# Optimization experiments

Measured on AMD Instinct MI355X. Metric: run time of the kernel, lower is better.

The kernel has to match this reference:

```python
import jax, jax.numpy as jnp
from jax import lax
import numpy as np

T, K, KEND = 2048, 4, 8
D, H, WD = 100, 256, 300
V, DICT, C = 20000, 700000, 18


def _build_end_indexed(starts, lens, ids, valid):
    # Group gazetteer words by their END position (the step at which the
    # lattice char cell consumes the word memory cell), padded to KEND slots.
    e_ids = np.zeros((T, KEND), np.int32)
    e_start = np.zeros((T, KEND), np.int32)
    e_mask = np.zeros((T, KEND), np.int32)
    cnt = np.zeros(T, np.int64)
    for t in range(T):
        for k in range(K):
            if valid[t, k]:
                e = int(starts[t, k] + lens[t, k] - 1)
                if cnt[e] < KEND:
                    e_ids[e, cnt[e]] = ids[t, k]
                    e_start[e, cnt[e]] = starts[t, k]
                    e_mask[e, cnt[e]] = 1
                    cnt[e] += 1
    return jnp.asarray(e_ids), jnp.asarray(e_start), jnp.asarray(e_mask)


def setup_inputs():
    ks = jax.random.split(jax.random.key(0), 24)
    inputs = jax.random.randint(ks[0], (1, T), 0, V, dtype=jnp.int32)
    rng = np.random.default_rng(0)
    lens = rng.integers(0, 8, size=(T, K))          # word length; valid iff >= 2
    ids = rng.integers(1, DICT, size=(T, K))        # gazetteer word ids
    pos = np.broadcast_to(np.arange(T)[:, None], (T, K))
    # forward direction: word starts at t, ends at t+len-1
    valid_f = (lens >= 2) & (pos + lens - 1 < T)
    fw_ids, fw_start, fw_mask = _build_end_indexed(pos, lens, ids, valid_f)
    # backward direction, expressed in the flipped frame: start' = T-1-(t+len-1)
    starts_b = T - 1 - (pos + lens - 1)
    valid_b = (lens >= 2) & (starts_b >= 0)
    bw_ids, bw_start, bw_mask = _build_end_indexed(starts_b, lens, ids, valid_b)
    s = 0.08
    nrm = lambda k, shape: jax.random.normal(k, shape, jnp.float32) * s
    p = {}
    i = 1
    for pre in ("fw", "bw"):
        p[pre + "_W_ih"] = nrm(ks[i], (D, 3 * H)); i += 1
        p[pre + "_W_hh"] = nrm(ks[i], (H, 3 * H)); i += 1
        p[pre + "_b"] = jnp.zeros((3 * H,), jnp.float32)
        p[pre + "_aW_ih"] = nrm(ks[i], (D, H)); i += 1
        p[pre + "_aW_hh"] = nrm(ks[i], (H, H)); i += 1
        p[pre + "_ab"] = jnp.zeros((H,), jnp.float32)
        p[pre + "_wW_ih"] = nrm(ks[i], (WD, 3 * H)); i += 1
        p[pre + "_wW_hh"] = nrm(ks[i], (H, 3 * H)); i += 1
        p[pre + "_wb"] = jnp.zeros((3 * H,), jnp.float32)
    out = dict(inputs=inputs, fw_ids=fw_ids, fw_start=fw_start, fw_mask=fw_mask,
               bw_ids=bw_ids, bw_start=bw_start, bw_mask=bw_mask, length=T,
               E=nrm(ks[20], (V, D)), word_table=nrm(ks[21], (DICT, WD)),
               W_lin=nrm(ks[22], (2 * H, C)), b_lin=jnp.zeros((C,), jnp.float32))
    out.update(p)
    return out


def _lattice_pass(x, wemb, start, mask, W_ih, W_hh, b, aW_ih, aW_hh, ab, wW_ih, wW_hh, wb):
    # x: [T,D]; wemb: [T,KEND,WD]; start/mask: [T,KEND]
    Tn, Hn = x.shape[0], W_hh.shape[0]

    def step(carry, xs):
        h, c, Hh, Ch = carry                        # Hh/Ch: [T,H] history of char states
        t, xt, we_t, st, m = xs
        mf = m.astype(x.dtype)[:, None]             # [KEND,1]
        hs, cs = Hh[st], Ch[st]                     # char state at each word's start pos
        # WordLSTMCell: c^w = sigmoid(f)*c_start + sigmoid(i)*tanh(g)
        wi, wf, wg = jnp.split(we_t @ wW_ih + hs @ wW_hh + wb, 3, axis=-1)
        cw = jax.nn.sigmoid(wf) * cs + jax.nn.sigmoid(wi) * jnp.tanh(wg)
        # MultiInputLSTMCell char gates
        ii, oo, gg = jnp.split(xt @ W_ih + h @ W_hh + b, 3, axis=-1)
        i_s, o_s, g_t = jax.nn.sigmoid(ii), jax.nn.sigmoid(oo), jnp.tanh(gg)
        # extra input gate per word, then exp-normalization over {i, alphas}
        alpha = jax.nn.sigmoid(xt @ aW_ih + cw @ aW_hh + ab)   # [KEND,H]
        e_i = jnp.exp(i_s)                                      # [H]
        e_a = jnp.exp(alpha) * mf                               # masked slots drop out
        c_merge = (e_i * g_t + (e_a * cw).sum(0)) / (e_i + e_a.sum(0))
        c_plain = (1.0 - i_s) * c + i_s * g_t                   # no-word branch (f = 1-i)
        c_new = jnp.where(jnp.any(m > 0), c_merge, c_plain)
        h_new = o_s * jnp.tanh(c_new)
        return (h_new, c_new, Hh.at[t].set(h_new), Ch.at[t].set(c_new)), h_new

    z = lambda *sh: jnp.zeros(sh, x.dtype)
    init = (z(Hn), z(Hn), z(Tn, Hn), z(Tn, Hn))
    _, hseq = lax.scan(step, init, (jnp.arange(Tn), x, wemb, start, mask))
    return hseq                                      # [T,H]


def reference(inputs, fw_ids, fw_start, fw_mask, bw_ids, bw_start, bw_mask, length, E,
              word_table, W_lin, b_lin,
              fw_W_ih, fw_W_hh, fw_b, fw_aW_ih, fw_aW_hh, fw_ab, fw_wW_ih, fw_wW_hh, fw_wb,
              bw_W_ih, bw_W_hh, bw_b, bw_aW_ih, bw_aW_hh, bw_ab, bw_wW_ih, bw_wW_hh, bw_wb):
    x = E[inputs[0]]                                 # [T,D] char embeddings (batch=1)
    hf = _lattice_pass(x, word_table[fw_ids], fw_start, fw_mask,
                       fw_W_ih, fw_W_hh, fw_b, fw_aW_ih, fw_aW_hh, fw_ab,
                       fw_wW_ih, fw_wW_hh, fw_wb)
    hb = _lattice_pass(x[::-1], word_table[bw_ids], bw_start, bw_mask,
                       bw_W_ih, bw_W_hh, bw_b, bw_aW_ih, bw_aW_hh, bw_ab,
                       bw_wW_ih, bw_wW_hh, bw_wb)[::-1]
    return (jnp.concatenate([hf, hb], axis=-1) @ W_lin + b_lin)[None]  # [1,T,C]
```

## Files before the change

### kernel.cpp

```cpp
#include <hip/hip_runtime.h>
#include <hip/hip_bf16.h>


#define TSEQ 2048
#define KEND 8
#define DEMB 100
#define H    256
#define H3   768
#define WD   300
#define CCLS 18
#define NTH  256

typedef __attribute__((ext_vector_type(8))) short bf16x8;
typedef __attribute__((ext_vector_type(4))) float f32x4;

#define LO_AT  0
#define LO_A1  131072
#define LO_VS  131584
#define LO_UR  133120
#define LO_RC  143872
#define LO_A2  152064
#define LO_AWS 156288
#define LO_MT  160384
#define SMEM_SCAN 160640

__device__ __forceinline__ float sigf(float x) { return 1.0f / (1.0f + expf(-x)); }
__device__ __forceinline__ float bf2f(unsigned u) { return __uint_as_float(u << 16); }
__device__ __forceinline__ unsigned f2bf(float f) {
  union { float f; unsigned u; } x; x.f = f;
  unsigned r = x.u + 0x7fffu + ((x.u >> 16) & 1u);
  return r >> 16;
}

__global__ __launch_bounds__(64) void k_pack(
    const float* __restrict__ W_hh_f, const float* __restrict__ wW_hh_f, const float* __restrict__ aW_hh_f,
    const float* __restrict__ W_hh_b, const float* __restrict__ wW_hh_b, const float* __restrict__ aW_hh_b,
    unsigned short* __restrict__ Wpk)
{
  const int T = blockIdx.x, dir = blockIdx.y;
  const int lane = threadIdx.x;
  const float* Wg = dir ? W_hh_b  : W_hh_f;
  const float* Ww = dir ? wW_hh_b : wW_hh_f;
  const float* Wa = dir ? aW_hh_b : aW_hh_f;
  for (int ks = 0; ks < 8; ++ks) {
    bf16x8 sv;
#pragma unroll
    for (int e = 0; e < 8; ++e) {
      const int k = ks * 32 + (lane >> 4) * 8 + e;
      float f;
      if (T < 96) {
        const int c = T * 16 + (lane & 15);
        f = (c < H3) ? Wg[(size_t)k * H3 + c] : Ww[(size_t)k * H3 + (c - H3)];
      } else {
        const int c = (T - 96) * 16 + (lane & 15);
        f = Wa[(size_t)k * H + c];
      }
      sv[e] = (short)f2bf(f);
    }
    *(bf16x8*)(Wpk + (((size_t)dir * 112 + T) * 8 + ks) * 512 + lane * 8) = sv;
  }
}

__global__ __launch_bounds__(256) void k_embed(
    const int* __restrict__ inputs, const float* __restrict__ E,
    const float* __restrict__ W_ih_f, const float* __restrict__ b_f,
    const float* __restrict__ aW_ih_f, const float* __restrict__ ab_f,
    const float* __restrict__ W_ih_b, const float* __restrict__ b_b,
    const float* __restrict__ aW_ih_b, const float* __restrict__ ab_b,
    __hip_bfloat16* __restrict__ xg, float* __restrict__ xa)
{
  const int t = blockIdx.x, dir = blockIdx.y;
  const int tid = threadIdx.x;
  const float* W_ih = dir ? W_ih_b : W_ih_f;
  const float* bb   = dir ? b_b    : b_f;
  const float* aW   = dir ? aW_ih_b : aW_ih_f;
  const float* ab   = dir ? ab_b   : ab_f;
  const int src = dir ? (TSEQ - 1 - t) : t;

  __shared__ float xr[DEMB];
  if (tid < DEMB) xr[tid] = E[(size_t)inputs[src] * DEMB + tid];
  __syncthreads();

  float a0 = bb[tid], a1 = bb[H + tid], a2 = bb[2 * H + tid], a3 = ab[tid];
  for (int r = 0; r < DEMB; r += 4) {
    const float4 e4 = *reinterpret_cast<const float4*>(&xr[r]);
    const float ev[4] = {e4.x, e4.y, e4.z, e4.w};
#pragma unroll
    for (int kk = 0; kk < 4; ++kk) {
      const float* wp = W_ih + (size_t)(r + kk) * H3 + tid;
      a0 += ev[kk] * wp[0];
      a1 += ev[kk] * wp[H];
      a2 += ev[kk] * wp[2 * H];
      a3 += ev[kk] * aW[(size_t)(r + kk) * H + tid];
    }
  }
  __hip_bfloat16* xgrow = xg + ((size_t)dir * TSEQ + t) * H3;
  xgrow[tid]         = __float2bfloat16(a0);
  xgrow[H + tid]     = __float2bfloat16(a1);
  xgrow[2 * H + tid] = __float2bfloat16(a2);
  xa[((size_t)dir * TSEQ + t) * H + tid] = a3;
}

__global__ __launch_bounds__(256) void k_wordgates(
    const int* __restrict__ fw_ids, const int* __restrict__ fw_mask,
    const int* __restrict__ bw_ids, const int* __restrict__ bw_mask,
    const float* __restrict__ word_table,
    const float* __restrict__ wW_ih_f, const float* __restrict__ wb_f,
    const float* __restrict__ wW_ih_b, const float* __restrict__ wb_b,
    __hip_bfloat16* __restrict__ wg)
{
  const int t = blockIdx.x, dir = blockIdx.y;
  const int tid = threadIdx.x;
  const int* ids = (dir ? bw_ids : fw_ids) + t * KEND;
  const int* msk = (dir ? bw_mask : fw_mask) + t * KEND;
  const float* wW = dir ? wW_ih_b : wW_ih_f;
  const float* wb = dir ? wb_b    : wb_f;

  __shared__ float we[KEND][WD];
  for (int w = 0; w < KEND; ++w) {
    if (msk[w]) {
      const float* src = word_table + (size_t)ids[w] * WD;
      for (int i = tid; i < WD; i += 256) we[w][i] = src[i];
    }
  }
  __syncthreads();

  __hip_bfloat16* out = wg + ((size_t)dir * TSEQ + t) * KEND * H3;
  for (int w = 0; w < KEND; ++w) {
    if (!msk[w]) continue;
    float a0 = wb[tid], a1 = wb[H + tid], a2 = wb[2 * H + tid];
    for (int r = 0; r < WD; r += 4) {
      const float4 e4 = *reinterpret_cast<const float4*>(&we[w][r]);
      const float ev[4] = {e4.x, e4.y, e4.z, e4.w};
#pragma unroll
      for (int kk = 0; kk < 4; ++kk) {
        const float* wp = wW + (size_t)(r + kk) * H3 + tid;
        a0 += ev[kk] * wp[0];
        a1 += ev[kk] * wp[H];
        a2 += ev[kk] * wp[2 * H];
      }
    }
    out[w * H3 + tid]         = __float2bfloat16(a0);
    out[w * H3 + H + tid]     = __float2bfloat16(a1);
    out[w * H3 + 2 * H + tid] = __float2bfloat16(a2);
  }
}

__global__ __launch_bounds__(NTH, 1) void k_scan(
    const __hip_bfloat16* __restrict__ xg, const float* __restrict__ xa,
    const __hip_bfloat16* __restrict__ wgG, float* __restrict__ hseq,
    const int* __restrict__ fw_start, const int* __restrict__ fw_mask,
    const int* __restrict__ bw_start, const int* __restrict__ bw_mask,
    const unsigned short* __restrict__ Wpk,
    unsigned long long* __restrict__ xb, unsigned* __restrict__ xf)
{
  const int gid = blockIdx.x;
  if (gid != 0 && gid != 1 && gid != 8 && gid != 9) return;
  const int dir  = gid & 1;
  const int side = gid >> 3;

  extern __shared__ char smem[];
  unsigned short* A1_16 = (unsigned short*)(smem + LO_A1);
  unsigned short* vS16  = (unsigned short*)(smem + LO_VS);
  unsigned short* ur16  = (unsigned short*)(smem + LO_UR);
  float* ringC = (float*)(smem + LO_RC);
  unsigned short* awS16 = (unsigned short*)(smem + LO_AWS);
  int* metaI = (int*)(smem + LO_MT);

  const int tid  = threadIdx.x;
  const int lane = tid & 63;
  const int wv   = tid >> 6;
  const int lmod = lane & 15;
  const int lgrp = lane >> 4;

  const int* startA = dir ? bw_start : fw_start;
  const int* maskA  = dir ? bw_mask  : fw_mask;
  const char* WpkD = (const char*)(Wpk + (size_t)dir * 112 * 8 * 512);

  unsigned long long* myPay = xb + (size_t)((dir * 2 + side) * 2) * 192;
  const unsigned long long* peerPay = xb + (size_t)((dir * 2 + (side ^ 1)) * 2) * 192;
  unsigned* myFlag   = xf + (dir * 2 + side) * 32;
  unsigned* peerFlag = xf + (dir * 2 + (side ^ 1)) * 32;

  bf16x8 rW[12][8];
  {
    const char* rp = WpkD + (size_t)(side * 48 + wv * 12) * 8192 + lane * 16;
#pragma unroll
    for (int n = 0; n < 12; ++n)
#pragma unroll
      for (int ks = 0; ks < 8; ++ks)
        rW[n][ks] = *(const bf16x8*)(rp + (n * 8 + ks) * 1024);
  }
  for (int o = tid * 16; o < 131072; o += NTH * 16)
    *(uint4*)(smem + LO_AT + o) = *(const uint4*)(WpkD + (size_t)96 * 8192 + o);
  if (tid < 32) *(uint4*)(smem + LO_A1 + tid * 16) = uint4{0, 0, 0, 0};
  for (int o = tid * 16; o < 4224; o += NTH * 16)
    *(uint4*)(smem + LO_A2 + o) = uint4{0, 0, 0, 0};
  for (int o = tid * 16; o < 8192; o += NTH * 16)
    *(uint4*)(smem + LO_RC + o) = uint4{0, 0, 0, 0};

  unsigned nxI = 0, nxO = 0, nxG = 0; float nxA = 0.f;
  unsigned cxI = 0, cxO = 0, cxG = 0; float cxA = 0.f;
  int nmt = 0;
  {
    const unsigned short* xr = (const unsigned short*)(xg + (size_t)dir * TSEQ * H3);
    nxI = xr[tid]; nxO = xr[H + tid]; nxG = xr[2 * H + tid];
    nxA = xa[(size_t)dir * TSEQ * H + tid];
    if (wv == 3) {
      if (lane < 8) nmt = maskA[lane];
      else if (lane < 16) nmt = startA[lane - 8];
    }
  }
  __syncthreads();
  if (wv == 3) {
    int mAll[8], sAll[8];
#pragma unroll
    for (int s = 0; s < 8; ++s) { mAll[s] = __shfl(nmt, s); sAll[s] = __shfl(nmt, 8 + s); }
    if (lane == 0) {
      int n = 0;
      for (int s = 0; s < 8; ++s)
        if (mAll[s]) { metaI[1 + n] = s; metaI[9 + n] = sAll[s]; ++n; }
      metaI[0] = n;
    }
  }
  cxI = nxI; cxO = nxO; cxG = nxG; cxA = nxA;
  __syncthreads();

  for (int t = 0; t < TSEQ; ++t) {
    const int par = t & 1;
    const int* mp = metaI + par * 32;
    const int nw = mp[0];
    const int us7 = (t + 6) % 7;
    unsigned short* stage16 = side ? (ur16 + us7 * 768) : vS16;
    unsigned short* rcv16   = side ? vS16 : (ur16 + us7 * 768);
    int hasL2w = 0;
    for (int w = 0; w < nw; ++w) hasL2w |= (mp[9 + w] == t - 1);

    unsigned short wgv[24];
#pragma unroll
    for (int it = 0; it < 8; ++it) {
      const int u0 = tid + it * NTH;
      if (u0 < nw * 256) {
        const int w = u0 >> 8, j = u0 & 255;
        const int slot = mp[1 + w];
        const unsigned short* wgp =
            (const unsigned short*)wgG + ((size_t)(dir * TSEQ + t) * KEND + slot) * H3 + j;
        wgv[it * 3 + 0] = wgp[0];
        wgv[it * 3 + 1] = wgp[256];
        wgv[it * 3 + 2] = wgp[512];
      }
    }

#pragma unroll
    for (int g = 0; g < 2; ++g) {
      f32x4 acc[6];
#pragma unroll
      for (int n = 0; n < 6; ++n) acc[n] = f32x4{0.f, 0.f, 0.f, 0.f};
#pragma unroll
      for (int ks = 0; ks < 8; ++ks) {
        const bf16x8 av = *(const bf16x8*)(smem + LO_A1 + ks * 64 + lgrp * 16);
#pragma unroll
        for (int n = 0; n < 6; ++n)
          acc[n] = __builtin_amdgcn_mfma_f32_16x16x32_bf16(av, rW[g * 6 + n][ks], acc[n], 0, 0, 0);
      }
      if (lane < 16) {
#pragma unroll
        for (int n = 0; n < 6; ++n)
          stage16[(wv * 12 + g * 6 + n) * 16 + lane] = (unsigned short)f2bf(acc[n][0]);
      }
    }
    __syncthreads();

    if (tid < 192) {
      const unsigned long long q = *(const unsigned long long*)((const char*)stage16 + tid * 8);
      __hip_atomic_store(myPay + par * 192 + tid, q, __ATOMIC_RELAXED, __HIP_MEMORY_SCOPE_AGENT);
    }
    __syncthreads();

    if (tid == 0)
      __hip_atomic_store(myFlag, (unsigned)(t + 1), __ATOMIC_RELAXED, __HIP_MEMORY_SCOPE_AGENT);

    {
      const int tn = (t + 1 < TSEQ) ? t + 1 : TSEQ - 1;
      const unsigned short* xr = (const unsigned short*)(xg + ((size_t)dir * TSEQ + tn) * H3);
      nxI = xr[tid]; nxO = xr[H + tid]; nxG = xr[2 * H + tid];
      nxA = xa[((size_t)dir * TSEQ + tn) * H + tid];
      if (wv == 3) {
        if (lane < 8) nmt = maskA[tn * KEND + lane];
        else if (lane < 16) nmt = startA[tn * KEND + (lane - 8)];
      }
    }
#pragma unroll
    for (int it = 0; it < 8; ++it) {
      const int u0 = tid + it * NTH;
      if (u0 < nw * 256) {
        const int w = u0 >> 8, j = u0 & 255;
        const int s = mp[9 + w];
        if (side == 1 || s != t - 1) {
          const unsigned short* ur = ur16 + (s % 7) * 768;
          const float wi  = bf2f(wgv[it * 3 + 0]) + bf2f(ur[j]);
          const float wf  = bf2f(wgv[it * 3 + 1]) + bf2f(ur[256 + j]);
          const float wgg = bf2f(wgv[it * 3 + 2]) + bf2f(ur[512 + j]);
          const float cs  = ringC[(s & 7) * 256 + j];
          const float cv  = sigf(wf) * cs + sigf(wi) * tanhf(wgg);
          *(unsigned short*)(smem + LO_A2 + w * 528 + j * 2) = (unsigned short)f2bf(cv);
        }
      }
    }
    if (nw > 0) {
      __syncthreads();

      {
        const int r2 = (lmod > 7) ? 7 : lmod;
        f32x4 ac[4];
#pragma unroll
        for (int m = 0; m < 4; ++m) ac[m] = f32x4{0.f, 0.f, 0.f, 0.f};
#pragma unroll
        for (int ks = 0; ks < 8; ++ks) {
          const bf16x8 a2v = *(const bf16x8*)(smem + LO_A2 + r2 * 528 + ks * 64 + lgrp * 16);
#pragma unroll
          for (int m = 0; m < 4; ++m) {
            const bf16x8 b = *(const bf16x8*)(smem + LO_AT + (size_t)(wv * 4 + m) * 8192 + ks * 1024 + lane * 16);
            ac[m] = __builtin_amdgcn_mfma_f32_16x16x32_bf16(a2v, b, ac[m], 0, 0, 0);
          }
        }
#pragma unroll
        for (int m = 0; m < 4; ++m) {
#pragma unroll
          for (int r = 0; r < 4; ++r) {
            const int row = lgrp * 4 + r;
            if (row < nw && mp[9 + row] != t - 1)
              awS16[row * 256 + (wv * 4 + m) * 16 + lmod] = (unsigned short)f2bf(ac[m][r]);
          }
        }
      }
    }

    if (tid == 0) {
      while (__hip_atomic_load(peerFlag, __ATOMIC_RELAXED, __HIP_MEMORY_SCOPE_AGENT) < (unsigned)(t + 1)) {}
    }
    __syncthreads();

    if (tid < 192) {
      const unsigned long long q =
          __hip_atomic_load(peerPay + par * 192 + tid, __ATOMIC_RELAXED, __HIP_MEMORY_SCOPE_AGENT);
      *(unsigned long long*)((char*)rcv16 + tid * 8) = q;
    }
    __syncthreads();

    if (hasL2w) {
      if (side == 0) {
#pragma unroll
        for (int it = 0; it < 8; ++it) {
          const int u0 = tid + it * NTH;
          if (u0 < nw * 256) {
            const int w = u0 >> 8, j = u0 & 255;
            const int s = mp[9 + w];
            if (s == t - 1) {
              const unsigned short* ur = ur16 + (s % 7) * 768;
              const float wi  = bf2f(wgv[it * 3 + 0]) + bf2f(ur[j]);
              const float wf  = bf2f(wgv[it * 3 + 1]) + bf2f(ur[256 + j]);
              const float wgg = bf2f(wgv[it * 3 + 2]) + bf2f(ur[512 + j]);
              const float cs  = ringC[(s & 7) * 256 + j];
              const float cv  = sigf(wf) * cs + sigf(wi) * tanhf(wgg);
              *(unsigned short*)(smem + LO_A2 + w * 528 + j * 2) = (unsigned short)f2bf(cv);
            }
          }
        }
      }
      __syncthreads();

      {
        const int r2 = (lmod > 7) ? 7 : lmod;
        f32x4 ac[4];
#pragma unroll
        for (int m = 0; m < 4; ++m) ac[m] = f32x4{0.f, 0.f, 0.f, 0.f};
#pragma unroll
        for (int ks = 0; ks < 8; ++ks) {
          const bf16x8 a2v = *(const bf16x8*)(smem + LO_A2 + r2 * 528 + ks * 64 + lgrp * 16);
#pragma unroll
          for (int m = 0; m < 4; ++m) {
            const bf16x8 b = *(const bf16x8*)(smem + LO_AT + (size_t)(wv * 4 + m) * 8192 + ks * 1024 + lane * 16);
            ac[m] = __builtin_amdgcn_mfma_f32_16x16x32_bf16(a2v, b, ac[m], 0, 0, 0);
          }
        }
#pragma unroll
        for (int m = 0; m < 4; ++m) {
#pragma unroll
          for (int r = 0; r < 4; ++r) {
            const int row = lgrp * 4 + r;
            if (row < nw && mp[9 + row] == t - 1)
              awS16[row * 256 + (wv * 4 + m) * 16 + lmod] = (unsigned short)f2bf(ac[m][r]);
          }
        }
      }
      __syncthreads();
    }

    {
      const int j = tid;
      const float i_s = sigf(bf2f(cxI) + bf2f(vS16[j]));
      const float o_s = sigf(bf2f(cxO) + bf2f(vS16[256 + j]));
      const float g_t = tanhf(bf2f(cxG) + bf2f(vS16[512 + j]));
      float cnew;
      if (nw > 0) {
        const float e_i = expf(i_s);
        float num = e_i * g_t, den = e_i;
        for (int w = 0; w < nw; ++w) {
          const float a  = sigf(cxA + bf2f(awS16[w * 256 + j]));
          const float ea = expf(a);
          num += ea * bf2f(*(const unsigned short*)(smem + LO_A2 + w * 528 + j * 2));
          den += ea;
        }
        cnew = num / den;
      } else {
        cnew = (1.f - i_s) * ringC[((t - 1) & 7) * 256 + j] + i_s * g_t;
      }
      const float hnew = o_s * tanhf(cnew);
      ringC[(t & 7) * 256 + j] = cnew;
      A1_16[j] = (unsigned short)f2bf(hnew);
      if ((side == 0) == (j < 128))
        hseq[((size_t)dir * TSEQ + t) * H + j] = hnew;
    }
    if (wv == 3) {
      int mAll[8], sAll[8];
#pragma unroll
      for (int s = 0; s < 8; ++s) { mAll[s] = __shfl(nmt, s); sAll[s] = __shfl(nmt, 8 + s); }
      if (lane == 0) {
        int* mq = metaI + ((t + 1) & 1) * 32;
        int n = 0;
        for (int s = 0; s < 8; ++s)
          if (mAll[s]) { mq[1 + n] = s; mq[9 + n] = sAll[s]; ++n; }
        mq[0] = n;
      }
    }
    cxI = nxI; cxO = nxO; cxG = nxG; cxA = nxA;
    __syncthreads();
  }
}

__global__ __launch_bounds__(64) void k_proj(
    const float* __restrict__ hseq, const float* __restrict__ W_lin,
    const float* __restrict__ b_lin, float* __restrict__ out)
{
  const int t = blockIdx.x;
  const int tid = threadIdx.x;
  __shared__ float hrow[2 * H];
  for (int i = tid; i < H; i += 64) {
    hrow[i]     = hseq[(size_t)t * H + i];
    hrow[H + i] = hseq[((size_t)TSEQ + (TSEQ - 1 - t)) * H + i];
  }
  __syncthreads();
  if (tid < CCLS) {
    float acc = b_lin[tid];
    for (int j = 0; j < 2 * H; ++j) acc += hrow[j] * W_lin[(size_t)j * CCLS + tid];
    out[(size_t)t * CCLS + tid] = acc;
  }
}

extern "C" void kernel_launch(void* const* d_in, const int* in_sizes, int n_in,
                              void* d_out, int out_size, void* d_ws, size_t ws_size,
                              hipStream_t stream)
{
  const int* inputs   = (const int*)d_in[0];
  const int* fw_ids   = (const int*)d_in[1];
  const int* fw_start = (const int*)d_in[2];
  const int* fw_mask  = (const int*)d_in[3];
  const int* bw_ids   = (const int*)d_in[4];
  const int* bw_start = (const int*)d_in[5];
  const int* bw_mask  = (const int*)d_in[6];
  const float* E          = (const float*)d_in[8];
  const float* word_table = (const float*)d_in[9];
  const float* W_lin      = (const float*)d_in[10];
  const float* b_lin      = (const float*)d_in[11];
  const float* fw_W_ih  = (const float*)d_in[12];
  const float* fw_W_hh  = (const float*)d_in[13];
  const float* fw_b     = (const float*)d_in[14];
  const float* fw_aW_ih = (const float*)d_in[15];
  const float* fw_aW_hh = (const float*)d_in[16];
  const float* fw_ab    = (const float*)d_in[17];
  const float* fw_wW_ih = (const float*)d_in[18];
  const float* fw_wW_hh = (const float*)d_in[19];
  const float* fw_wb    = (const float*)d_in[20];
  const float* bw_W_ih  = (const float*)d_in[21];
  const float* bw_W_hh  = (const float*)d_in[22];
  const float* bw_b     = (const float*)d_in[23];
  const float* bw_aW_ih = (const float*)d_in[24];
  const float* bw_aW_hh = (const float*)d_in[25];
  const float* bw_ab    = (const float*)d_in[26];
  const float* bw_wW_ih = (const float*)d_in[27];
  const float* bw_wW_hh = (const float*)d_in[28];
  const float* bw_wb    = (const float*)d_in[29];

  char* p = (char*)d_ws;
  __hip_bfloat16* xg = (__hip_bfloat16*)p;  p += (size_t)2 * TSEQ * H3 * 2;
  float* xa   = (float*)p;                  p += (size_t)2 * TSEQ * H * 4;
  float* hseq = (float*)p;                  p += (size_t)2 * TSEQ * H * 4;
  __hip_bfloat16* wg = (__hip_bfloat16*)p;  p += (size_t)2 * TSEQ * KEND * H3 * 2;
  unsigned short* Wpk = (unsigned short*)p; p += (size_t)2 * 112 * 8 * 512 * 2;
  unsigned long long* xb = (unsigned long long*)p; p += (size_t)2 * 2 * 2 * 192 * 8;
  unsigned* xf = (unsigned*)p;              p += 512;

  hipFuncSetAttribute((const void*)k_scan,
                      hipFuncAttributeMaxDynamicSharedMemorySize, SMEM_SCAN);
  hipMemsetAsync(xf, 0, 512, stream);

  k_pack<<<dim3(112, 2), 64, 0, stream>>>(
      fw_W_hh, fw_wW_hh, fw_aW_hh, bw_W_hh, bw_wW_hh, bw_aW_hh, Wpk);
  k_embed<<<dim3(TSEQ, 2), 256, 0, stream>>>(
      inputs, E, fw_W_ih, fw_b, fw_aW_ih, fw_ab, bw_W_ih, bw_b, bw_aW_ih, bw_ab, xg, xa);
  k_wordgates<<<dim3(TSEQ, 2), 256, 0, stream>>>(
      fw_ids, fw_mask, bw_ids, bw_mask, word_table, fw_wW_ih, fw_wb, bw_wW_ih, bw_wb, wg);
  k_scan<<<16, NTH, SMEM_SCAN, stream>>>(
      xg, xa, wg, hseq, fw_start, fw_mask, bw_start, bw_mask, Wpk, xb, xf);
  k_proj<<<TSEQ, 64, 0, stream>>>(hseq, W_lin, b_lin, (float*)d_out);
}
```

Measured before the change: 16.80 ms.

## Replace flag-based cross-block handshake with sequence-tagged payload words

Each payload word now carries the step number in its upper 32 bits, so the receiving block spins on the data words themselves rather than on a separate flag followed by a second read. This removes the staging barrier, the separate flag store and the extra syncthreads. The word-cell work is also split by side: side 1 computes all word cells before waiting on its peer, and side 0 computes the cells it can before waiting. The cost is doubled payload traffic, since each 64-bit word now holds 32 bits of data, plus per-thread spinning on 384 words.

```diff
diff --git a/kernel.cpp b/kernel.cpp
--- a/kernel.cpp
+++ b/kernel.cpp
@@ -152,7 +152,7 @@
     const int* __restrict__ fw_start, const int* __restrict__ fw_mask,
     const int* __restrict__ bw_start, const int* __restrict__ bw_mask,
     const unsigned short* __restrict__ Wpk,
-    unsigned long long* __restrict__ xb, unsigned* __restrict__ xf)
+    unsigned long long* __restrict__ xb)
 {
   const int gid = blockIdx.x;
   if (gid != 0 && gid != 1 && gid != 8 && gid != 9) return;
@@ -177,10 +177,8 @@
   const int* maskA  = dir ? bw_mask  : fw_mask;
   const char* WpkD = (const char*)(Wpk + (size_t)dir * 112 * 8 * 512);
 
-  unsigned long long* myPay = xb + (size_t)((dir * 2 + side) * 2) * 192;
-  const unsigned long long* peerPay = xb + (size_t)((dir * 2 + (side ^ 1)) * 2) * 192;
-  unsigned* myFlag   = xf + (dir * 2 + side) * 32;
-  unsigned* peerFlag = xf + (dir * 2 + (side ^ 1)) * 32;
+  unsigned long long* myPay = xb + (size_t)((dir * 2 + side) * 2) * 384;
+  const unsigned long long* peerPay = xb + (size_t)((dir * 2 + (side ^ 1)) * 2) * 384;
 
   bf16x8 rW[12][8];
   {
@@ -233,8 +231,6 @@
     const int us7 = (t + 6) % 7;
     unsigned short* stage16 = side ? (ur16 + us7 * 768) : vS16;
     unsigned short* rcv16   = side ? vS16 : (ur16 + us7 * 768);
-    int hasL2w = 0;
-    for (int w = 0; w < nw; ++w) hasL2w |= (mp[9 + w] == t - 1);
 
     unsigned short wgv[24];
 #pragma unroll
@@ -263,22 +259,23 @@
         for (int n = 0; n < 6; ++n)
           acc[n] = __builtin_amdgcn_mfma_f32_16x16x32_bf16(av, rW[g * 6 + n][ks], acc[n], 0, 0, 0);
       }
-      if (lane < 16) {
-#pragma unroll
-        for (int n = 0; n < 6; ++n)
-          stage16[(wv * 12 + g * 6 + n) * 16 + lane] = (unsigned short)f2bf(acc[n][0]);
-      }
-    }
-    __syncthreads();
-
-    if (tid < 192) {
-      const unsigned long long q = *(const unsigned long long*)((const char*)stage16 + tid * 8);
-      __hip_atomic_store(myPay + par * 192 + tid, q, __ATOMIC_RELAXED, __HIP_MEMORY_SCOPE_AGENT);
-    }
-    __syncthreads();
-
-    if (tid == 0)
-      __hip_atomic_store(myFlag, (unsigned)(t + 1), __ATOMIC_RELAXED, __HIP_MEMORY_SCOPE_AGENT);
+#pragma unroll
+      for (int n = 0; n < 6; ++n) {
+        const unsigned hb = f2bf(acc[n][0]) & 0xffffu;
+        const unsigned ob = (unsigned)__shfl_down((int)hb, 1) & 0xffffu;
+        if (lane < 16) {
+          const int tix = wv * 12 + g * 6 + n;
+          stage16[tix * 16 + lane] = (unsigned short)hb;
+          if (!(lane & 1)) {
+            const unsigned long long q =
+                ((unsigned long long)(unsigned)(t + 1) << 32) |
+                (unsigned long long)(hb | (ob << 16));
+            __hip_atomic_store(myPay + par * 384 + tix * 8 + (lane >> 1), q,
+                               __ATOMIC_RELAXED, __HIP_MEMORY_SCOPE_AGENT);
+          }
+        }
+      }
+    }
 
     {
       const int tn = (t + 1 < TSEQ) ? t + 1 : TSEQ - 1;
@@ -290,66 +287,39 @@
         else if (lane < 16) nmt = startA[tn * KEND + (lane - 8)];
       }
     }
-#pragma unroll
-    for (int it = 0; it < 8; ++it) {
-      const int u0 = tid + it * NTH;
-      if (u0 < nw * 256) {
-        const int w = u0 >> 8, j = u0 & 255;
-        const int s = mp[9 + w];
-        if (side == 1 || s != t - 1) {
-          const unsigned short* ur = ur16 + (s % 7) * 768;
-          const float wi  = bf2f(wgv[it * 3 + 0]) + bf2f(ur[j]);
-          const float wf  = bf2f(wgv[it * 3 + 1]) + bf2f(ur[256 + j]);
-          const float wgg = bf2f(wgv[it * 3 + 2]) + bf2f(ur[512 + j]);
-          const float cs  = ringC[(s & 7) * 256 + j];
-          const float cv  = sigf(wf) * cs + sigf(wi) * tanhf(wgg);
-          *(unsigned short*)(smem + LO_A2 + w * 528 + j * 2) = (unsigned short)f2bf(cv);
-        }
-      }
-    }
-    if (nw > 0) {
+    __syncthreads();
+
+    if (side == 0) {
+      if (nw > 0) {
+#pragma unroll
+        for (int it = 0; it < 8; ++it) {
+          const int u0 = tid + it * NTH;
+          if (u0 < nw * 256) {
+            const int w = u0 >> 8, j = u0 & 255;
+            const int s = mp[9 + w];
+            if (s != t - 1) {
+              const unsigned short* ur = ur16 + (s % 7) * 768;
+              const float wi  = bf2f(wgv[it * 3 + 0]) + bf2f(ur[j]);
+              const float wf  = bf2f(wgv[it * 3 + 1]) + bf2f(ur[256 + j]);
+              const float wgg = bf2f(wgv[it * 3 + 2]) + bf2f(ur[512 + j]);
+              const float cs  = ringC[(s & 7) * 256 + j];
+              const float cv  = sigf(wf) * cs + sigf(wi) * tanhf(wgg);
+              *(unsigned short*)(smem + LO_A2 + w * 528 + j * 2) = (unsigned short)f2bf(cv);
+            }
+          }
+        }
+      }
+      if (tid < 192) {
+        unsigned long long q;
+        do { q = __hip_atomic_load(peerPay + par * 384 + tid, __ATOMIC_RELAXED, __HIP_MEMORY_SCOPE_AGENT); }
+        while ((unsigned)(q >> 32) != (unsigned)(t + 1));
+        *(unsigned*)((char*)rcv16 + tid * 4) = (unsigned)q;
+        do { q = __hip_atomic_load(peerPay + par * 384 + 192 + tid, __ATOMIC_RELAXED, __HIP_MEMORY_SCOPE_AGENT); }
+        while ((unsigned)(q >> 32) != (unsigned)(t + 1));
+        *(unsigned*)((char*)rcv16 + (192 + tid) * 4) = (unsigned)q;
+      }
       __syncthreads();
-
-      {
-        const int r2 = (lmod > 7) ? 7 : lmod;
-        f32x4 ac[4];
-#pragma unroll
-        for (int m = 0; m < 4; ++m) ac[m] = f32x4{0.f, 0.f, 0.f, 0.f};
-#pragma unroll
-        for (int ks = 0; ks < 8; ++ks) {
-          const bf16x8 a2v = *(const bf16x8*)(smem + LO_A2 + r2 * 528 + ks * 64 + lgrp * 16);
-#pragma unroll
-          for (int m = 0; m < 4; ++m) {
-            const bf16x8 b = *(const bf16x8*)(smem + LO_AT + (size_t)(wv * 4 + m) * 8192 + ks * 1024 + lane * 16);
-            ac[m] = __builtin_amdgcn_mfma_f32_16x16x32_bf16(a2v, b, ac[m], 0, 0, 0);
-          }
-        }
-#pragma unroll
-        for (int m = 0; m < 4; ++m) {
-#pragma unroll
-          for (int r = 0; r < 4; ++r) {
-            const int row = lgrp * 4 + r;
-            if (row < nw && mp[9 + row] != t - 1)
-              awS16[row * 256 + (wv * 4 + m) * 16 + lmod] = (unsigned short)f2bf(ac[m][r]);
-          }
-        }
-      }
-    }
-
-    if (tid == 0) {
-      while (__hip_atomic_load(peerFlag, __ATOMIC_RELAXED, __HIP_MEMORY_SCOPE_AGENT) < (unsigned)(t + 1)) {}
-    }
-    __syncthreads();
-
-    if (tid < 192) {
-      const unsigned long long q =
-          __hip_atomic_load(peerPay + par * 192 + tid, __ATOMIC_RELAXED, __HIP_MEMORY_SCOPE_AGENT);
-      *(unsigned long long*)((char*)rcv16 + tid * 8) = q;
-    }
-    __syncthreads();
-
-    if (hasL2w) {
-      if (side == 0) {
+      if (nw > 0) {
 #pragma unroll
         for (int it = 0; it < 8; ++it) {
           const int u0 = tid + it * NTH;
@@ -367,32 +337,80 @@
             }
           }
         }
-      }
-      __syncthreads();
-
-      {
-        const int r2 = (lmod > 7) ? 7 : lmod;
-        f32x4 ac[4];
-#pragma unroll
-        for (int m = 0; m < 4; ++m) ac[m] = f32x4{0.f, 0.f, 0.f, 0.f};
-#pragma unroll
-        for (int ks = 0; ks < 8; ++ks) {
-          const bf16x8 a2v = *(const bf16x8*)(smem + LO_A2 + r2 * 528 + ks * 64 + lgrp * 16);
-#pragma unroll
-          for (int m = 0; m < 4; ++m) {
-            const bf16x8 b = *(const bf16x8*)(smem + LO_AT + (size_t)(wv * 4 + m) * 8192 + ks * 1024 + lane * 16);
-            ac[m] = __builtin_amdgcn_mfma_f32_16x16x32_bf16(a2v, b, ac[m], 0, 0, 0);
+        __syncthreads();
+        {
+          const int r2 = (lmod > 7) ? 7 : lmod;
+          f32x4 ac[4];
+#pragma unroll
+          for (int m = 0; m < 4; ++m) ac[m] = f32x4{0.f, 0.f, 0.f, 0.f};
+#pragma unroll
+          for (int ks = 0; ks < 8; ++ks) {
+            const bf16x8 a2v = *(const bf16x8*)(smem + LO_A2 + r2 * 528 + ks * 64 + lgrp * 16);
+#pragma unroll
+            for (int m = 0; m < 4; ++m) {
+              const bf16x8 b = *(const bf16x8*)(smem + LO_AT + (size_t)(wv * 4 + m) * 8192 + ks * 1024 + lane * 16);
+              ac[m] = __builtin_amdgcn_mfma_f32_16x16x32_bf16(a2v, b, ac[m], 0, 0, 0);
+            }
           }
-        }
-#pragma unroll
-        for (int m = 0; m < 4; ++m) {
-#pragma unroll
-          for (int r = 0; r < 4; ++r) {
-            const int row = lgrp * 4 + r;
-            if (row < nw && mp[9 + row] == t - 1)
-              awS16[row * 256 + (wv * 4 + m) * 16 + lmod] = (unsigned short)f2bf(ac[m][r]);
+#pragma unroll
+          for (int m = 0; m < 4; ++m)
+#pragma unroll
+            for (int r = 0; r < 4; ++r) {
+              const int row = lgrp * 4 + r;
+              if (row < nw) awS16[row * 256 + (wv * 4 + m) * 16 + lmod] = (unsigned short)f2bf(ac[m][r]);
+            }
+        }
+        __syncthreads();
+      }
+    } else {
+      if (nw > 0) {
+#pragma unroll
+        for (int it = 0; it < 8; ++it) {
+          const int u0 = tid + it * NTH;
+          if (u0 < nw * 256) {
+            const int w = u0 >> 8, j = u0 & 255;
+            const int s = mp[9 + w];
+            const unsigned short* ur = ur16 + (s % 7) * 768;
+            const float wi  = bf2f(wgv[it * 3 + 0]) + bf2f(ur[j]);
+            const float wf  = bf2f(wgv[it * 3 + 1]) + bf2f(ur[256 + j]);
+            const float wgg = bf2f(wgv[it * 3 + 2]) + bf2f(ur[512 + j]);
+            const float cs  = ringC[(s & 7) * 256 + j];
+            const float cv  = sigf(wf) * cs + sigf(wi) * tanhf(wgg);
+            *(unsigned short*)(smem + LO_A2 + w * 528 + j * 2) = (unsigned short)f2bf(cv);
           }
         }
+        __syncthreads();
+        {
+          const int r2 = (lmod > 7) ? 7 : lmod;
+          f32x4 ac[4];
+#pragma unroll
+          for (int m = 0; m < 4; ++m) ac[m] = f32x4{0.f, 0.f, 0.f, 0.f};
+#pragma unroll
+          for (int ks = 0; ks < 8; ++ks) {
+            const bf16x8 a2v = *(const bf16x8*)(smem + LO_A2 + r2 * 528 + ks * 64 + lgrp * 16);
+#pragma unroll
+            for (int m = 0; m < 4; ++m) {
+              const bf16x8 b = *(const bf16x8*)(smem + LO_AT + (size_t)(wv * 4 + m) * 8192 + ks * 1024 + lane * 16);
+              ac[m] = __builtin_amdgcn_mfma_f32_16x16x32_bf16(a2v, b, ac[m], 0, 0, 0);
+            }
+          }
+#pragma unroll
+          for (int m = 0; m < 4; ++m)
+#pragma unroll
+            for (int r = 0; r < 4; ++r) {
+              const int row = lgrp * 4 + r;
+              if (row < nw) awS16[row * 256 + (wv * 4 + m) * 16 + lmod] = (unsigned short)f2bf(ac[m][r]);
+            }
+        }
+      }
+      if (tid < 192) {
+        unsigned long long q;
+        do { q = __hip_atomic_load(peerPay + par * 384 + tid, __ATOMIC_RELAXED, __HIP_MEMORY_SCOPE_AGENT); }
+        while ((unsigned)(q >> 32) != (unsigned)(t + 1));
+        *(unsigned*)((char*)rcv16 + tid * 4) = (unsigned)q;
+        do { q = __hip_atomic_load(peerPay + par * 384 + 192 + tid, __ATOMIC_RELAXED, __HIP_MEMORY_SCOPE_AGENT); }
+        while ((unsigned)(q >> 32) != (unsigned)(t + 1));
+        *(unsigned*)((char*)rcv16 + (192 + tid) * 4) = (unsigned)q;
       }
       __syncthreads();
     }
@@ -498,12 +516,13 @@
   float* hseq = (float*)p;                  p += (size_t)2 * TSEQ * H * 4;
   __hip_bfloat16* wg = (__hip_bfloat16*)p;  p += (size_t)2 * TSEQ * KEND * H3 * 2;
   unsigned short* Wpk = (unsigned short*)p; p += (size_t)2 * 112 * 8 * 512 * 2;
-  unsigned long long* xb = (unsigned long long*)p; p += (size_t)2 * 2 * 2 * 192 * 8;
-  unsigned* xf = (unsigned*)p;              p += 512;
+  unsigned long long* xb = (unsigned long long*)p;
+  const size_t xb_bytes = (size_t)2 * 2 * 2 * 384 * 8;
+  p += xb_bytes;
 
   hipFuncSetAttribute((const void*)k_scan,
                       hipFuncAttributeMaxDynamicSharedMemorySize, SMEM_SCAN);
-  hipMemsetAsync(xf, 0, 512, stream);
+  hipMemsetAsync(xb, 0, xb_bytes, stream);
 
   k_pack<<<dim3(112, 2), 64, 0, stream>>>(
       fw_W_hh, fw_wW_hh, fw_aW_hh, bw_W_hh, bw_wW_hh, bw_aW_hh, Wpk);
@@ -512,6 +531,6 @@
   k_wordgates<<<dim3(TSEQ, 2), 256, 0, stream>>>(
       fw_ids, fw_mask, bw_ids, bw_mask, word_table, fw_wW_ih, fw_wb, bw_wW_ih, bw_wb, wg);
   k_scan<<<16, NTH, SMEM_SCAN, stream>>>(
-      xg, xa, wg, hseq, fw_start, fw_mask, bw_start, bw_mask, Wpk, xb, xf);
+      xg, xa, wg, hseq, fw_start, fw_mask, bw_start, bw_mask, Wpk, xb);
   k_proj<<<TSEQ, 64, 0, stream>>>(hseq, W_lin, b_lin, (float*)d_out);
 }
```

Result: slower. 17.31 ms (+3.0%).
